# Kernel tuning notes

Hardware: AMD Instinct MI355X
Metric: run time of the kernel (lower is better)

The kernel has to match this reference:

```python
import jax, jax.numpy as jnp
import numpy as np

E, D, H, O, K = 12, 1024, 2048, 1024, 4
HH, G1, G2 = H // 2, 256, 128
B = 4096


def _ln(x, g, b):
    # torch LayerNorm over last dim, eps=1e-5
    m = x.mean(-1, keepdims=True)
    v = ((x - m) ** 2).mean(-1, keepdims=True)
    return (x - m) * jax.lax.rsqrt(v + 1e-5) * g + b


def setup_inputs() -> dict:
    key = jax.random.key(0)
    ks = jax.random.split(key, 12)
    s = 0.02
    f32 = jnp.float32
    return {
        "x": jax.random.normal(ks[0], (B, D), f32),
        # stacked expert params (E experts)
        "ew_in": jax.random.normal(ks[1], (E, D, H), f32) * s,
        "eb_in": jnp.full((E, H), 0.1, f32),
        "ln1_g": jnp.ones((E, H), f32),
        "ln1_b": jnp.zeros((E, H), f32),
        "ew_h1": jax.random.normal(ks[2], (E, H, H), f32) * s,
        "eb_h1": jnp.full((E, H), 0.1, f32),
        "ln2_g": jnp.ones((E, H), f32),
        "ln2_b": jnp.zeros((E, H), f32),
        "ew_h2": jax.random.normal(ks[3], (E, H, HH), f32) * s,
        "eb_h2": jnp.full((E, HH), 0.1, f32),
        "ew_out": jax.random.normal(ks[4], (E, HH, O), f32) * s,
        "eb_out": jnp.zeros((E, O), f32),
        # gating network params
        "gw_in": jax.random.normal(ks[5], (D, G1), f32) * s,
        "gb_in": jnp.zeros((G1,), f32),
        "gln1_g": jnp.ones((G1,), f32),
        "gln1_b": jnp.zeros((G1,), f32),
        "gw_1": jax.random.normal(ks[6], (G1, G1), f32) * s,
        "gb_1": jnp.full((G1,), 0.1, f32),
        "gln2_g": jnp.ones((G1,), f32),
        "gln2_b": jnp.zeros((G1,), f32),
        "gw_2": jax.random.normal(ks[7], (G1, G2), f32) * s,
        "gb_2": jnp.full((G2,), 0.1, f32),
        "gw_out": jax.random.normal(ks[8], (G2, E), f32) * s,
        "gb_out": jnp.zeros((E,), f32),
        "temperature": jnp.ones((1,), f32),
    }


def _moe(x, ew_in, eb_in, ln1_g, ln1_b, ew_h1, eb_h1, ln2_g, ln2_b, ew_h2,
         eb_h2, ew_out, eb_out, gw_in, gb_in, gln1_g, gln1_b, gw_1, gb_1,
         gln2_g, gln2_b, gw_2, gb_2, gw_out, gb_out, temperature):
    # ---- gating network (eval mode: no dropout / noise) ----
    g0 = jax.nn.relu(x @ gw_in + gb_in)                                # [B,256]
    g1 = jax.nn.relu(_ln(g0, gln1_g, gln1_b)) @ gw_1 + gb_1 + g0       # residual
    g2 = jax.nn.relu(_ln(g1, gln2_g, gln2_b)) @ gw_2 + gb_2            # [B,128]
    logits = (g2 @ gw_out + gb_out) / temperature                      # [B,E]
    probs = jax.nn.softmax(logits, axis=1)
    topp, topi = jax.lax.top_k(probs, K)                               # [B,K]
    topp = topp / topp.sum(axis=1, keepdims=True)
    # ---- experts: batched over E, combined with top-k one-hot weights ----
    h0 = jax.nn.relu(jnp.einsum('bd,edh->ebh', x, ew_in) + eb_in[:, None, :])
    a1 = jax.nn.relu(_ln(h0, ln1_g[:, None, :], ln1_b[:, None, :]))
    h1 = jnp.einsum('ebh,ehg->ebg', a1, ew_h1) + eb_h1[:, None, :] + h0
    a2 = jax.nn.silu(_ln(h1, ln2_g[:, None, :], ln2_b[:, None, :]))
    h2 = jnp.einsum('ebh,ehm->ebm', a2, ew_h2) + eb_h2[:, None, :]     # [E,B,H/2]
    y = jnp.einsum('ebm,emo->ebo', h2, ew_out) + eb_out[:, None, :]    # [E,B,O]
    oh = jax.nn.one_hot(topi, E, dtype=probs.dtype)                    # [B,K,E]
    w = jnp.einsum('bk,bke->be', topp, oh)                             # combine weights
    final = jnp.einsum('be,ebo->bo', w, y)                             # [B,O]
    # ---- load-balancing loss (eval-mode path) ----
    usage = probs.mean(axis=0)                                         # [E]
    ideal = 1.0 / E
    kl = jnp.sum(ideal * (jnp.log(ideal) - jnp.log(usage + 1e-8)))
    var = jnp.sum((usage - ideal) ** 2)
    ent = -jnp.sum(usage * jnp.log(usage + 1e-8))
    ent_loss = 1.0 - ent / np.log(E).astype(np.float32)
    loss = (0.5 * kl + 0.3 * var + 0.2 * ent_loss) * 0.05
    return final, loss, probs


def reference(x, ew_in, eb_in, ln1_g, ln1_b, ew_h1, eb_h1, ln2_g, ln2_b,
              ew_h2, eb_h2, ew_out, eb_out, gw_in, gb_in, gln1_g, gln1_b,
              gw_1, gb_1, gln2_g, gln2_b, gw_2, gb_2, gw_out, gb_out,
              temperature):
    return _moe(x, ew_in, eb_in, ln1_g, ln1_b, ew_h1, eb_h1, ln2_g, ln2_b,
                ew_h2, eb_h2, ew_out, eb_out, gw_in, gb_in, gln1_g, gln1_b,
                gw_1, gb_1, gln2_g, gln2_b, gw_2, gb_2, gw_out, gb_out,
                temperature)
```

## Files before the change

kernel.cpp:

```cpp
#include <hip/hip_runtime.h>
#include <cstdint>
#include <cstddef>

typedef __bf16 bf16;
typedef __bf16 bf16x4 __attribute__((ext_vector_type(4)));
typedef __bf16 bf16x8 __attribute__((ext_vector_type(8)));
typedef float  f32x4  __attribute__((ext_vector_type(4)));

#define NE   12
#define DDIM 1024
#define HDIM 2048
#define MDIM 1024
#define ODIM 1024
#define GG1  256
#define GG2  128
#define BB   4096
#define ROWS_MAX 18432

#define GPTR(p) ((const __attribute__((address_space(1))) void*)(p))
#define LPTR(p) ((__attribute__((address_space(3))) void*)(p))

__global__ void cvt_f32_bf16(const float* __restrict__ in, bf16* __restrict__ out) {
    size_t i = ((size_t)blockIdx.x * 256 + threadIdx.x) * 4;
    float4 v = *(const float4*)(in + i);
    bf16x4 o = { (bf16)v.x, (bf16)v.y, (bf16)v.z, (bf16)v.w };
    *(bf16x4*)(out + i) = o;
}

__global__ __launch_bounds__(256)
void transpose_cvt(const float* __restrict__ in, bf16* __restrict__ out,
                   int K, int N) {
    __shared__ float tile[64][65];
    const size_t eo = (size_t)blockIdx.z * K * N;
    in  += eo;
    out += eo;
    const int n0 = blockIdx.x * 64, k0 = blockIdx.y * 64;
    const int tid = threadIdx.x;

    const int rkk = tid >> 4, rnc = (tid & 15) * 4;
    #pragma unroll
    for (int p = 0; p < 4; ++p) {
        const int kk = p * 16 + rkk;
        const float4 v = *(const float4*)(in + (size_t)(k0 + kk) * N + n0 + rnc);
        tile[kk][rnc] = v.x; tile[kk][rnc + 1] = v.y;
        tile[kk][rnc + 2] = v.z; tile[kk][rnc + 3] = v.w;
    }
    __syncthreads();

    const int wnn = tid >> 3, wkc = (tid & 7) * 8;
    #pragma unroll
    for (int p = 0; p < 2; ++p) {
        const int nn = p * 32 + wnn;
        bf16x8 o;
        #pragma unroll
        for (int j = 0; j < 8; ++j) o[j] = (bf16)tile[wkc + j][nn];
        *(bf16x8*)(out + (size_t)(n0 + nn) * K + k0 + wkc) = o;
    }
}

__global__ void route_init(int* __restrict__ tok2slot, int* __restrict__ lists,
                           int* __restrict__ counts, int* __restrict__ cursors) {
    const int i = blockIdx.x * 256 + threadIdx.x;
    if (i < BB * NE)   tok2slot[i] = -1;
    if (i < ROWS_MAX)  lists[i] = 0;
    if (i < NE)        { counts[i] = 0; cursors[i] = 0; }
}

__global__ void route_count(const float* __restrict__ wcomb, int* __restrict__ counts) {
    const int t = blockIdx.x * 256 + threadIdx.x;
    const int e = blockIdx.y;
    if (wcomb[(size_t)t * NE + e] > 0.f) atomicAdd(&counts[e], 1);
}

__global__ void route_offsets(const int* __restrict__ counts, int* __restrict__ offs) {
    if (threadIdx.x == 0) {
        int o = 0;
        for (int e = 0; e < NE; ++e) { offs[e] = o; o += (counts[e] + 127) & ~127; }
        offs[NE] = o;
    }
}

__global__ void route_assign(const float* __restrict__ wcomb, const int* __restrict__ offs,
                             int* __restrict__ cursors, int* __restrict__ lists,
                             int* __restrict__ tok2slot) {
    const int t = blockIdx.x * 256 + threadIdx.x;
    const int e = blockIdx.y;
    if (wcomb[(size_t)t * NE + e] > 0.f) {
        const int pos  = atomicAdd(&cursors[e], 1);
        const int slot = offs[e] + pos;
        lists[slot] = t;
        tok2slot[(size_t)t * NE + e] = slot;
    }
}

__global__ void gather_rows(const bf16* __restrict__ xb, const int* __restrict__ lists,
                            const int* __restrict__ offs, bf16* __restrict__ xg) {
    const int e = blockIdx.y, p = blockIdx.x;
    const int off = offs[e];
    if (p >= offs[e + 1] - off) return;
    const int slot = off + p;
    const int t = lists[slot];
    const int tid = threadIdx.x;
    *(bf16x8*)&xg[(size_t)slot * DDIM + tid * 8] =
        *(const bf16x8*)&xb[(size_t)t * DDIM + tid * 8];
}

__global__ void combine_out(const int* __restrict__ tok2slot, const float* __restrict__ wcomb,
                            const float* __restrict__ yc, float* __restrict__ out) {
    const int t = blockIdx.x, tid = threadIdx.x;
    float4 acc = { 0.f, 0.f, 0.f, 0.f };
    #pragma unroll
    for (int e = 0; e < NE; ++e) {
        const int s = tok2slot[(size_t)t * NE + e];
        if (s >= 0) {
            const float w = wcomb[(size_t)t * NE + e];
            const float4 y = *(const float4*)&yc[(size_t)s * ODIM + tid * 4];
            acc.x += w * y.x; acc.y += w * y.y; acc.z += w * y.z; acc.w += w * y.w;
        }
    }
    *(float4*)&out[(size_t)t * ODIM + tid * 4] = acc;
}

template<int EPI>
__global__ __launch_bounds__(256, 2)
void egemm(const bf16* __restrict__ A, const bf16* __restrict__ Wt,
           const float* __restrict__ bias, const bf16* __restrict__ res,
           bf16* __restrict__ Cb, float* __restrict__ Cf,
           const int* __restrict__ offs, int N, int K)
{
    const int e = blockIdx.z;
    const int off  = offs[e];
    const int cntp = offs[e + 1] - off;
    const int m0 = blockIdx.y * 128;
    if (m0 >= cntp) return;
    const int n0 = blockIdx.x * 128;

    __shared__ bf16 sA[3][128 * 32];
    __shared__ bf16 sB[3][128 * 32];
    const int tid  = threadIdx.x;
    const int lane = tid & 63;
    const int wave = tid >> 6;
    const int wr = wave >> 1, wc = wave & 1;
    const int q  = lane >> 4;
    const int lr = lane & 15;

    const bf16*  Ae  = A + (size_t)off * K;
    const bf16*  Wte = Wt + (size_t)e * N * K;
    const float* be  = bias + (size_t)e * N;

    const bf16* srcA[2];
    const bf16* srcB[2];
    int dsto[2];
    #pragma unroll
    for (int i = 0; i < 2; ++i) {
        const int ch  = i * 256 + tid;
        const int row = ch >> 2, c = ch & 3;
        const int qg  = c ^ ((row >> 1) & 3);
        srcA[i] = Ae  + (size_t)(m0 + row) * K + qg * 8;
        srcB[i] = Wte + (size_t)(n0 + row) * K + qg * 8;
        dsto[i] = (i * 256 + (tid & 192)) * 8;
    }

    f32x4 acc[4][4] = {};

    auto stage = [&](int buf, int kt) {
        const int k0 = kt << 5;
        #pragma unroll
        for (int i = 0; i < 2; ++i) {
            __builtin_amdgcn_global_load_lds(GPTR(srcA[i] + k0), LPTR(&sA[buf][dsto[i]]), 16, 0, 0);
            __builtin_amdgcn_global_load_lds(GPTR(srcB[i] + k0), LPTR(&sB[buf][dsto[i]]), 16, 0, 0);
        }
    };

    const int NT = K >> 5;
    stage(0, 0);
    stage(1, 1);

    for (int kt = 0; kt < NT; ++kt) {
        const int cur = kt % 3;
        if (kt + 1 < NT) { asm volatile("s_waitcnt vmcnt(4)" ::: "memory"); }
        else             { asm volatile("s_waitcnt vmcnt(0)" ::: "memory"); }
        __builtin_amdgcn_sched_barrier(0);
        __builtin_amdgcn_s_barrier();
        __builtin_amdgcn_sched_barrier(0);

        bf16x8 fa[4], fb[4];
        #pragma unroll
        for (int mi = 0; mi < 4; ++mi) {
            const int r = wr * 64 + mi * 16 + lr;
            const int c = q ^ ((r >> 1) & 3);
            fa[mi] = *(const bf16x8*)&sA[cur][(size_t)(r * 4 + c) * 8];
        }
        #pragma unroll
        for (int ni = 0; ni < 4; ++ni) {
            const int r = wc * 64 + ni * 16 + lr;
            const int c = q ^ ((r >> 1) & 3);
            fb[ni] = *(const bf16x8*)&sB[cur][(size_t)(r * 4 + c) * 8];
        }
        #pragma unroll
        for (int mi = 0; mi < 4; ++mi)
            #pragma unroll
            for (int ni = 0; ni < 4; ++ni)
                acc[mi][ni] = __builtin_amdgcn_mfma_f32_16x16x32_bf16(fa[mi], fb[ni], acc[mi][ni], 0, 0, 0);

        if (kt + 2 < NT) stage((kt + 2) % 3, kt + 2);
    }

    #pragma unroll
    for (int ni = 0; ni < 4; ++ni) {
        const int c  = n0 + wc * 64 + ni * 16 + lr;
        const float bv = be[c];
        #pragma unroll
        for (int mi = 0; mi < 4; ++mi) {
            const int rloc = wr * 64 + mi * 16 + q * 4;
            #pragma unroll
            for (int j = 0; j < 4; ++j) {
                const size_t idx = (size_t)(off + m0 + rloc + j) * N + c;
                float v = acc[mi][ni][j] + bv;
                if constexpr (EPI == 0)      { Cb[idx] = (bf16)fmaxf(v, 0.f); }
                else if constexpr (EPI == 1) { Cb[idx] = (bf16)(v + (float)res[idx]); }
                else if constexpr (EPI == 2) { Cb[idx] = (bf16)v; }
                else                         { Cf[idx] = v; }
            }
        }
    }
}

template<int ACT>
__global__ __launch_bounds__(256)
void ln_act_bf16(const bf16* __restrict__ in, const float* __restrict__ gam,
                 const float* __restrict__ bet, bf16* __restrict__ out,
                 const int* __restrict__ offs)
{
    const int e = blockIdx.y;
    const int row = blockIdx.x;
    const int off = offs[e];
    if (row >= offs[e + 1] - off) return;
    const int tid = threadIdx.x;
    const size_t base = (size_t)(off + row) * HDIM;
    const float* g = gam + (size_t)e * HDIM;
    const float* b = bet + (size_t)e * HDIM;
    bf16x8 v = *(const bf16x8*)(in + base + tid * 8);
    float x[8], s = 0.f, ss = 0.f;
    #pragma unroll
    for (int j = 0; j < 8; ++j) { x[j] = (float)v[j]; s += x[j]; ss += x[j] * x[j]; }
    #pragma unroll
    for (int o = 1; o < 64; o <<= 1) { s += __shfl_xor(s, o); ss += __shfl_xor(ss, o); }
    __shared__ float rs[4], rss[4];
    if ((tid & 63) == 0) { rs[tid >> 6] = s; rss[tid >> 6] = ss; }
    __syncthreads();
    s  = rs[0] + rs[1] + rs[2] + rs[3];
    ss = rss[0] + rss[1] + rss[2] + rss[3];
    const float mean = s * (1.f / HDIM);
    const float var  = ss * (1.f / HDIM) - mean * mean;
    const float rstd = rsqrtf(var + 1e-5f);
    bf16x8 ov;
    #pragma unroll
    for (int j = 0; j < 8; ++j) {
        const int col = tid * 8 + j;
        float y = (x[j] - mean) * rstd * g[col] + b[col];
        if constexpr (ACT == 0) y = fmaxf(y, 0.f);
        else                    y = y / (1.f + expf(-y));
        ov[j] = (bf16)y;
    }
    *(bf16x8*)(out + base + tid * 8) = ov;
}

template<int EPI>
__global__ __launch_bounds__(256)
void gemm_f32(const float* __restrict__ A, const float* __restrict__ Bm,
              const float* __restrict__ bias, const float* __restrict__ res,
              float* __restrict__ C, int M, int N, int K)
{
    __shared__ float As[64][17];
    __shared__ float Bs[16][64];
    const int tid = threadIdx.x;
    const int tx = tid & 15, ty = tid >> 4;
    const int n0 = blockIdx.x * 64, m0 = blockIdx.y * 64;
    float acc[4][4] = {};

    for (int k0 = 0; k0 < K; k0 += 16) {
        {
            const int r = tid >> 2, c = (tid & 3) * 4;
            const float4 va = *(const float4*)(A + (size_t)(m0 + r) * K + k0 + c);
            As[r][c] = va.x; As[r][c + 1] = va.y; As[r][c + 2] = va.z; As[r][c + 3] = va.w;
            const int rb = tid >> 4, cb = (tid & 15) * 4;
            *(float4*)&Bs[rb][cb] = *(const float4*)(Bm + (size_t)(k0 + rb) * N + n0 + cb);
        }
        __syncthreads();
        #pragma unroll
        for (int k = 0; k < 16; ++k) {
            const float4 b4 = *(const float4*)&Bs[k][tx * 4];
            float av[4];
            #pragma unroll
            for (int i = 0; i < 4; ++i) av[i] = As[ty * 4 + i][k];
            #pragma unroll
            for (int i = 0; i < 4; ++i) {
                acc[i][0] += av[i] * b4.x; acc[i][1] += av[i] * b4.y;
                acc[i][2] += av[i] * b4.z; acc[i][3] += av[i] * b4.w;
            }
        }
        __syncthreads();
    }

    const float4 b4 = *(const float4*)(bias + n0 + tx * 4);
    #pragma unroll
    for (int i = 0; i < 4; ++i) {
        const int r = m0 + ty * 4 + i;
        float o[4] = { acc[i][0] + b4.x, acc[i][1] + b4.y, acc[i][2] + b4.z, acc[i][3] + b4.w };
        if constexpr (EPI == 0) {
            #pragma unroll
            for (int j = 0; j < 4; ++j) o[j] = fmaxf(o[j], 0.f);
        } else if constexpr (EPI == 1) {
            const float4 r4 = *(const float4*)(res + (size_t)r * N + n0 + tx * 4);
            o[0] += r4.x; o[1] += r4.y; o[2] += r4.z; o[3] += r4.w;
        }
        float4 o4 = { o[0], o[1], o[2], o[3] };
        *(float4*)(C + (size_t)r * N + n0 + tx * 4) = o4;
    }
}

__global__ void ln_relu_f32_256(const float* __restrict__ in, const float* __restrict__ g,
                                const float* __restrict__ b, float* __restrict__ out)
{
    const int row = blockIdx.x, lane = threadIdx.x;
    const size_t base = (size_t)row * GG1;
    const float4 v = *(const float4*)(in + base + lane * 4);
    float s  = v.x + v.y + v.z + v.w;
    float ss = v.x * v.x + v.y * v.y + v.z * v.z + v.w * v.w;
    #pragma unroll
    for (int o = 1; o < 64; o <<= 1) { s += __shfl_xor(s, o); ss += __shfl_xor(ss, o); }
    const float mean = s * (1.f / GG1);
    const float var  = ss * (1.f / GG1) - mean * mean;
    const float rstd = rsqrtf(var + 1e-5f);
    const float4 g4 = *(const float4*)(g + lane * 4);
    const float4 b4 = *(const float4*)(b + lane * 4);
    float4 o4;
    o4.x = fmaxf((v.x - mean) * rstd * g4.x + b4.x, 0.f);
    o4.y = fmaxf((v.y - mean) * rstd * g4.y + b4.y, 0.f);
    o4.z = fmaxf((v.z - mean) * rstd * g4.z + b4.z, 0.f);
    o4.w = fmaxf((v.w - mean) * rstd * g4.w + b4.w, 0.f);
    *(float4*)(out + base + lane * 4) = o4;
}

__global__ void gate_head(const float* __restrict__ g2, const float* __restrict__ gwout,
                          const float* __restrict__ gbout, const float* __restrict__ temp,
                          float* __restrict__ probs_out, float* __restrict__ wout)
{
    const int row = blockIdx.x, lane = threadIdx.x;
    __shared__ float lg[NE];
    const int e = lane >> 2, part = lane & 3;
    float acc = 0.f;
    if (e < NE) {
        const float* gr = g2 + (size_t)row * GG2;
        #pragma unroll
        for (int i = 0; i < 32; ++i) {
            const int k = part * 32 + i;
            acc += gr[k] * gwout[(size_t)k * NE + e];
        }
    }
    acc += __shfl_xor(acc, 1);
    acc += __shfl_xor(acc, 2);
    if (e < NE && part == 0) lg[e] = acc + gbout[e];
    __syncthreads();
    if (lane == 0) {
        const float t = temp[0];
        float p[NE];
        float mx = -1e30f;
        #pragma unroll
        for (int i = 0; i < NE; ++i) { p[i] = lg[i] / t; mx = fmaxf(mx, p[i]); }
        float se = 0.f;
        #pragma unroll
        for (int i = 0; i < NE; ++i) { p[i] = expf(p[i] - mx); se += p[i]; }
        const float inv = 1.f / se;
        #pragma unroll
        for (int i = 0; i < NE; ++i) { p[i] *= inv; probs_out[(size_t)row * NE + i] = p[i]; }
        float qq[NE], w[NE];
        #pragma unroll
        for (int i = 0; i < NE; ++i) { qq[i] = p[i]; w[i] = 0.f; }
        float tv[4]; int ti[4]; float tsum = 0.f;
        for (int k = 0; k < 4; ++k) {
            int best = 0; float bv = qq[0];
            for (int i = 1; i < NE; ++i) if (qq[i] > bv) { bv = qq[i]; best = i; }
            tv[k] = bv; ti[k] = best; qq[best] = -1e30f; tsum += bv;
        }
        const float it = 1.f / tsum;
        for (int k = 0; k < 4; ++k) w[ti[k]] = tv[k] * it;
        #pragma unroll
        for (int i = 0; i < NE; ++i) wout[(size_t)row * NE + i] = w[i];
    }
}

__global__ void usage_mean(const float* __restrict__ probs, float* __restrict__ usage) {
    const int e = blockIdx.x, tid = threadIdx.x;
    float s = 0.f;
    for (int r = tid; r < BB; r += 256) s += probs[(size_t)r * NE + e];
    #pragma unroll
    for (int o = 1; o < 64; o <<= 1) s += __shfl_xor(s, o);
    __shared__ float ps[4];
    if ((tid & 63) == 0) ps[tid >> 6] = s;
    __syncthreads();
    if (tid == 0) usage[e] = (ps[0] + ps[1] + ps[2] + ps[3]) / (float)BB;
}

__global__ void loss_kernel(const float* __restrict__ usage, float* __restrict__ out_loss) {
    if (threadIdx.x == 0) {
        const float ideal = 1.f / 12.f;
        float kl = 0.f, var = 0.f, ent = 0.f;
        for (int e = 0; e < NE; ++e) {
            const float u = usage[e];
            kl  += ideal * (logf(ideal) - logf(u + 1e-8f));
            var += (u - ideal) * (u - ideal);
            ent -= u * logf(u + 1e-8f);
        }
        const float entl = 1.f - ent / logf(12.f);
        out_loss[0] = (0.5f * kl + 0.3f * var + 0.2f * entl) * 0.05f;
    }
}

extern "C" void kernel_launch(void* const* d_in, const int* in_sizes, int n_in,
                              void* d_out, int out_size, void* d_ws, size_t ws_size,
                              hipStream_t stream)
{
    const float* x      = (const float*)d_in[0];
    const float* ew_in  = (const float*)d_in[1];
    const float* eb_in  = (const float*)d_in[2];
    const float* ln1_g  = (const float*)d_in[3];
    const float* ln1_b  = (const float*)d_in[4];
    const float* ew_h1  = (const float*)d_in[5];
    const float* eb_h1  = (const float*)d_in[6];
    const float* ln2_g  = (const float*)d_in[7];
    const float* ln2_b  = (const float*)d_in[8];
    const float* ew_h2  = (const float*)d_in[9];
    const float* eb_h2  = (const float*)d_in[10];
    const float* ew_out = (const float*)d_in[11];
    const float* eb_out = (const float*)d_in[12];
    const float* gw_in  = (const float*)d_in[13];
    const float* gb_in  = (const float*)d_in[14];
    const float* gln1_g = (const float*)d_in[15];
    const float* gln1_b = (const float*)d_in[16];
    const float* gw_1   = (const float*)d_in[17];
    const float* gb_1   = (const float*)d_in[18];
    const float* gln2_g = (const float*)d_in[19];
    const float* gln2_b = (const float*)d_in[20];
    const float* gw_2   = (const float*)d_in[21];
    const float* gb_2   = (const float*)d_in[22];
    const float* gw_out = (const float*)d_in[23];
    const float* gb_out = (const float*)d_in[24];
    const float* temp   = (const float*)d_in[25];

    float* out_final = (float*)d_out;
    float* out_loss  = out_final + (size_t)BB * ODIM;
    float* out_probs = out_loss + 1;

    char* ws = (char*)d_ws;
    size_t off = 0;
    auto alloc = [&](size_t bytes) -> void* {
        void* p = ws + off;
        off += (bytes + 255) & ~(size_t)255;
        return p;
    };

    bf16* xb     = (bf16*)alloc((size_t)BB * DDIM * 2);
    bf16* wt_in  = (bf16*)alloc((size_t)NE * HDIM * DDIM * 2);
    bf16* wt_h1  = (bf16*)alloc((size_t)NE * HDIM * HDIM * 2);
    bf16* wt_h2  = (bf16*)alloc((size_t)NE * MDIM * HDIM * 2);
    bf16* wt_out = (bf16*)alloc((size_t)NE * ODIM * MDIM * 2);
    bf16* xg     = (bf16*)alloc((size_t)ROWS_MAX * DDIM * 2);
    bf16* regA   = (bf16*)alloc((size_t)ROWS_MAX * HDIM * 2);
    bf16* regB   = (bf16*)alloc((size_t)ROWS_MAX * HDIM * 2);
    bf16* h1     = (bf16*)alloc((size_t)ROWS_MAX * HDIM * 2);
    float* yc    = (float*)alloc((size_t)ROWS_MAX * ODIM * 4);
    bf16* h0 = regA; bf16* a2 = regA;
    bf16* a1 = regB; bf16* h2 = regB;
    float* g0    = (float*)alloc((size_t)BB * GG1 * 4);
    float* t1    = (float*)alloc((size_t)BB * GG1 * 4);
    float* g1    = (float*)alloc((size_t)BB * GG1 * 4);
    float* t2    = (float*)alloc((size_t)BB * GG1 * 4);
    float* g2b   = (float*)alloc((size_t)BB * GG2 * 4);
    float* wcomb = (float*)alloc((size_t)BB * NE * 4);
    int*   lists = (int*)alloc((size_t)ROWS_MAX * 4);
    int*   t2s   = (int*)alloc((size_t)BB * NE * 4);
    int*   counts= (int*)alloc(256);
    int*   curs  = (int*)alloc(256);
    int*   offs  = (int*)alloc(256);
    float* usage = (float*)alloc(256);

    cvt_f32_bf16<<<dim3(BB * DDIM / 1024), dim3(256), 0, stream>>>(x, xb);
    transpose_cvt<<<dim3(HDIM / 64, DDIM / 64, NE), dim3(256), 0, stream>>>(ew_in,  wt_in,  DDIM, HDIM);
    transpose_cvt<<<dim3(HDIM / 64, HDIM / 64, NE), dim3(256), 0, stream>>>(ew_h1,  wt_h1,  HDIM, HDIM);
    transpose_cvt<<<dim3(MDIM / 64, HDIM / 64, NE), dim3(256), 0, stream>>>(ew_h2,  wt_h2,  HDIM, MDIM);
    transpose_cvt<<<dim3(ODIM / 64, MDIM / 64, NE), dim3(256), 0, stream>>>(ew_out, wt_out, MDIM, ODIM);

    gemm_f32<0><<<dim3(GG1 / 64, BB / 64), dim3(256), 0, stream>>>(x,  gw_in, gb_in, nullptr, g0,  BB, GG1, DDIM);
    ln_relu_f32_256<<<dim3(BB), dim3(64), 0, stream>>>(g0, gln1_g, gln1_b, t1);
    gemm_f32<1><<<dim3(GG1 / 64, BB / 64), dim3(256), 0, stream>>>(t1, gw_1,  gb_1,  g0,      g1,  BB, GG1, GG1);
    ln_relu_f32_256<<<dim3(BB), dim3(64), 0, stream>>>(g1, gln2_g, gln2_b, t2);
    gemm_f32<2><<<dim3(GG2 / 64, BB / 64), dim3(256), 0, stream>>>(t2, gw_2,  gb_2,  nullptr, g2b, BB, GG2, GG1);
    gate_head<<<dim3(BB), dim3(64), 0, stream>>>(g2b, gw_out, gb_out, temp, out_probs, wcomb);
    usage_mean<<<dim3(NE), dim3(256), 0, stream>>>(out_probs, usage);
    loss_kernel<<<dim3(1), dim3(64), 0, stream>>>(usage, out_loss);

    route_init<<<dim3((BB * NE + 255) / 256), dim3(256), 0, stream>>>(t2s, lists, counts, curs);
    route_count<<<dim3(BB / 256, NE), dim3(256), 0, stream>>>(wcomb, counts);
    route_offsets<<<dim3(1), dim3(64), 0, stream>>>(counts, offs);
    route_assign<<<dim3(BB / 256, NE), dim3(256), 0, stream>>>(wcomb, offs, curs, lists, t2s);
    gather_rows<<<dim3(BB, NE), dim3(128), 0, stream>>>(xb, lists, offs, xg);

    egemm<0><<<dim3(HDIM / 128, BB / 128, NE), dim3(256), 0, stream>>>(
        xg, wt_in, eb_in, nullptr, h0, nullptr, offs, HDIM, DDIM);
    ln_act_bf16<0><<<dim3(BB, NE), dim3(256), 0, stream>>>(h0, ln1_g, ln1_b, a1, offs);
    egemm<1><<<dim3(HDIM / 128, BB / 128, NE), dim3(256), 0, stream>>>(
        a1, wt_h1, eb_h1, h0, h1, nullptr, offs, HDIM, HDIM);
    ln_act_bf16<1><<<dim3(BB, NE), dim3(256), 0, stream>>>(h1, ln2_g, ln2_b, a2, offs);
    egemm<2><<<dim3(MDIM / 128, BB / 128, NE), dim3(256), 0, stream>>>(
        a2, wt_h2, eb_h2, nullptr, h2, nullptr, offs, MDIM, HDIM);
    egemm<3><<<dim3(ODIM / 128, BB / 128, NE), dim3(256), 0, stream>>>(
        h2, wt_out, eb_out, nullptr, nullptr, yc, offs, ODIM, MDIM);

    combine_out<<<dim3(BB), dim3(256), 0, stream>>>(t2s, wcomb, yc, out_final);
}
```

Baseline: 896.6 us.

## Fuse token gather into expert GEMM, deepen LDS pipeline, split-K gating GEMM

Removes the separate gather kernel by having the first expert GEMM read input rows indirectly through the routing list. Increases the GEMM software pipeline from three to four LDS stages with adjusted waitcnt thresholds. Splits the first gating GEMM over K into two partial buffers, followed by a reduction kernel that adds bias and applies ReLU. The changes trade an extra LDS footprint, which may reduce occupancy, and one extra kernel launch for fewer global memory round trips and more latency hiding.

```diff
diff --git a/kernel.cpp b/kernel.cpp
--- a/kernel.cpp
+++ b/kernel.cpp
@@ -93,18 +93,6 @@
     }
 }
 
-__global__ void gather_rows(const bf16* __restrict__ xb, const int* __restrict__ lists,
-                            const int* __restrict__ offs, bf16* __restrict__ xg) {
-    const int e = blockIdx.y, p = blockIdx.x;
-    const int off = offs[e];
-    if (p >= offs[e + 1] - off) return;
-    const int slot = off + p;
-    const int t = lists[slot];
-    const int tid = threadIdx.x;
-    *(bf16x8*)&xg[(size_t)slot * DDIM + tid * 8] =
-        *(const bf16x8*)&xb[(size_t)t * DDIM + tid * 8];
-}
-
 __global__ void combine_out(const int* __restrict__ tok2slot, const float* __restrict__ wcomb,
                             const float* __restrict__ yc, float* __restrict__ out) {
     const int t = blockIdx.x, tid = threadIdx.x;
@@ -126,7 +114,8 @@
 void egemm(const bf16* __restrict__ A, const bf16* __restrict__ Wt,
            const float* __restrict__ bias, const bf16* __restrict__ res,
            bf16* __restrict__ Cb, float* __restrict__ Cf,
-           const int* __restrict__ offs, int N, int K)
+           const int* __restrict__ offs, const int* __restrict__ lists,
+           int N, int K)
 {
     const int e = blockIdx.z;
     const int off  = offs[e];
@@ -135,8 +124,8 @@
     if (m0 >= cntp) return;
     const int n0 = blockIdx.x * 128;
 
-    __shared__ bf16 sA[3][128 * 32];
-    __shared__ bf16 sB[3][128 * 32];
+    __shared__ bf16 sA[4][128 * 32];
+    __shared__ bf16 sB[4][128 * 32];
     const int tid  = threadIdx.x;
     const int lane = tid & 63;
     const int wave = tid >> 6;
@@ -144,7 +133,6 @@
     const int q  = lane >> 4;
     const int lr = lane & 15;
 
-    const bf16*  Ae  = A + (size_t)off * K;
     const bf16*  Wte = Wt + (size_t)e * N * K;
     const float* be  = bias + (size_t)e * N;
 
@@ -156,7 +144,10 @@
         const int ch  = i * 256 + tid;
         const int row = ch >> 2, c = ch & 3;
         const int qg  = c ^ ((row >> 1) & 3);
-        srcA[i] = Ae  + (size_t)(m0 + row) * K + qg * 8;
+        size_t arow;
+        if constexpr (EPI == 0) arow = (size_t)lists[off + m0 + row];
+        else                    arow = (size_t)(off + m0 + row);
+        srcA[i] = A   + arow * K + qg * 8;
         srcB[i] = Wte + (size_t)(n0 + row) * K + qg * 8;
         dsto[i] = (i * 256 + (tid & 192)) * 8;
     }
@@ -175,11 +166,14 @@
     const int NT = K >> 5;
     stage(0, 0);
     stage(1, 1);
+    stage(2, 2);
 
     for (int kt = 0; kt < NT; ++kt) {
-        const int cur = kt % 3;
-        if (kt + 1 < NT) { asm volatile("s_waitcnt vmcnt(4)" ::: "memory"); }
-        else             { asm volatile("s_waitcnt vmcnt(0)" ::: "memory"); }
+        const int cur = kt & 3;
+        const int rem = NT - kt;
+        if (rem >= 3)      { asm volatile("s_waitcnt vmcnt(8)" ::: "memory"); }
+        else if (rem == 2) { asm volatile("s_waitcnt vmcnt(4)" ::: "memory"); }
+        else               { asm volatile("s_waitcnt vmcnt(0)" ::: "memory"); }
         __builtin_amdgcn_sched_barrier(0);
         __builtin_amdgcn_s_barrier();
         __builtin_amdgcn_sched_barrier(0);
@@ -203,7 +197,7 @@
             for (int ni = 0; ni < 4; ++ni)
                 acc[mi][ni] = __builtin_amdgcn_mfma_f32_16x16x32_bf16(fa[mi], fb[ni], acc[mi][ni], 0, 0, 0);
 
-        if (kt + 2 < NT) stage((kt + 2) % 3, kt + 2);
+        if (kt + 3 < NT) stage((kt + 3) & 3, kt + 3);
     }
 
     #pragma unroll
@@ -318,6 +312,68 @@
         float4 o4 = { o[0], o[1], o[2], o[3] };
         *(float4*)(C + (size_t)r * N + n0 + tx * 4) = o4;
     }
+}
+
+__global__ __launch_bounds__(256)
+void gemm_f32_sk(const float* __restrict__ A, const float* __restrict__ Bm,
+                 float* __restrict__ Cp, int M, int N, int K)
+{
+    __shared__ float As[64][17];
+    __shared__ float Bs[16][64];
+    const int tid = threadIdx.x;
+    const int tx = tid & 15, ty = tid >> 4;
+    const int n0 = blockIdx.x * 64, m0 = blockIdx.y * 64;
+    const int kh = K >> 1;
+    const int kb = blockIdx.z * kh, ke = kb + kh;
+    float acc[4][4] = {};
+
+    for (int k0 = kb; k0 < ke; k0 += 16) {
+        {
+            const int r = tid >> 2, c = (tid & 3) * 4;
+            const float4 va = *(const float4*)(A + (size_t)(m0 + r) * K + k0 + c);
+            As[r][c] = va.x; As[r][c + 1] = va.y; As[r][c + 2] = va.z; As[r][c + 3] = va.w;
+            const int rb = tid >> 4, cb = (tid & 15) * 4;
+            *(float4*)&Bs[rb][cb] = *(const float4*)(Bm + (size_t)(k0 + rb) * N + n0 + cb);
+        }
+        __syncthreads();
+        #pragma unroll
+        for (int k = 0; k < 16; ++k) {
+            const float4 b4 = *(const float4*)&Bs[k][tx * 4];
+            float av[4];
+            #pragma unroll
+            for (int i = 0; i < 4; ++i) av[i] = As[ty * 4 + i][k];
+            #pragma unroll
+            for (int i = 0; i < 4; ++i) {
+                acc[i][0] += av[i] * b4.x; acc[i][1] += av[i] * b4.y;
+                acc[i][2] += av[i] * b4.z; acc[i][3] += av[i] * b4.w;
+            }
+        }
+        __syncthreads();
+    }
+
+    float* Cz = Cp + (size_t)blockIdx.z * M * N;
+    #pragma unroll
+    for (int i = 0; i < 4; ++i) {
+        const int r = m0 + ty * 4 + i;
+        float4 o4 = { acc[i][0], acc[i][1], acc[i][2], acc[i][3] };
+        *(float4*)(Cz + (size_t)r * N + n0 + tx * 4) = o4;
+    }
+}
+
+__global__ void sk_reduce_relu(const float* __restrict__ Cp, const float* __restrict__ bias,
+                               float* __restrict__ C)
+{
+    const size_t i = ((size_t)blockIdx.x * 256 + threadIdx.x) * 4;
+    const int col = (int)(i % GG1);
+    const float4 a = *(const float4*)(Cp + i);
+    const float4 b = *(const float4*)(Cp + (size_t)BB * GG1 + i);
+    const float4 bi = *(const float4*)(bias + col);
+    float4 o;
+    o.x = fmaxf(a.x + b.x + bi.x, 0.f);
+    o.y = fmaxf(a.y + b.y + bi.y, 0.f);
+    o.z = fmaxf(a.z + b.z + bi.z, 0.f);
+    o.w = fmaxf(a.w + b.w + bi.w, 0.f);
+    *(float4*)(C + i) = o;
 }
 
 __global__ void ln_relu_f32_256(const float* __restrict__ in, const float* __restrict__ g,
@@ -466,13 +522,13 @@
     bf16* wt_h1  = (bf16*)alloc((size_t)NE * HDIM * HDIM * 2);
     bf16* wt_h2  = (bf16*)alloc((size_t)NE * MDIM * HDIM * 2);
     bf16* wt_out = (bf16*)alloc((size_t)NE * ODIM * MDIM * 2);
-    bf16* xg     = (bf16*)alloc((size_t)ROWS_MAX * DDIM * 2);
     bf16* regA   = (bf16*)alloc((size_t)ROWS_MAX * HDIM * 2);
     bf16* regB   = (bf16*)alloc((size_t)ROWS_MAX * HDIM * 2);
     bf16* h1     = (bf16*)alloc((size_t)ROWS_MAX * HDIM * 2);
     float* yc    = (float*)alloc((size_t)ROWS_MAX * ODIM * 4);
     bf16* h0 = regA; bf16* a2 = regA;
     bf16* a1 = regB; bf16* h2 = regB;
+    float* skbuf = (float*)alloc((size_t)2 * BB * GG1 * 4);
     float* g0    = (float*)alloc((size_t)BB * GG1 * 4);
     float* t1    = (float*)alloc((size_t)BB * GG1 * 4);
     float* g1    = (float*)alloc((size_t)BB * GG1 * 4);
@@ -492,7 +548,8 @@
     transpose_cvt<<<dim3(MDIM / 64, HDIM / 64, NE), dim3(256), 0, stream>>>(ew_h2,  wt_h2,  HDIM, MDIM);
     transpose_cvt<<<dim3(ODIM / 64, MDIM / 64, NE), dim3(256), 0, stream>>>(ew_out, wt_out, MDIM, ODIM);
 
-    gemm_f32<0><<<dim3(GG1 / 64, BB / 64), dim3(256), 0, stream>>>(x,  gw_in, gb_in, nullptr, g0,  BB, GG1, DDIM);
+    gemm_f32_sk<<<dim3(GG1 / 64, BB / 64, 2), dim3(256), 0, stream>>>(x, gw_in, skbuf, BB, GG1, DDIM);
+    sk_reduce_relu<<<dim3(BB * GG1 / 1024), dim3(256), 0, stream>>>(skbuf, gb_in, g0);
     ln_relu_f32_256<<<dim3(BB), dim3(64), 0, stream>>>(g0, gln1_g, gln1_b, t1);
     gemm_f32<1><<<dim3(GG1 / 64, BB / 64), dim3(256), 0, stream>>>(t1, gw_1,  gb_1,  g0,      g1,  BB, GG1, GG1);
     ln_relu_f32_256<<<dim3(BB), dim3(64), 0, stream>>>(g1, gln2_g, gln2_b, t2);
@@ -505,18 +562,17 @@
     route_count<<<dim3(BB / 256, NE), dim3(256), 0, stream>>>(wcomb, counts);
     route_offsets<<<dim3(1), dim3(64), 0, stream>>>(counts, offs);
     route_assign<<<dim3(BB / 256, NE), dim3(256), 0, stream>>>(wcomb, offs, curs, lists, t2s);
-    gather_rows<<<dim3(BB, NE), dim3(128), 0, stream>>>(xb, lists, offs, xg);
 
     egemm<0><<<dim3(HDIM / 128, BB / 128, NE), dim3(256), 0, stream>>>(
-        xg, wt_in, eb_in, nullptr, h0, nullptr, offs, HDIM, DDIM);
+        xb, wt_in, eb_in, nullptr, h0, nullptr, offs, lists, HDIM, DDIM);
     ln_act_bf16<0><<<dim3(BB, NE), dim3(256), 0, stream>>>(h0, ln1_g, ln1_b, a1, offs);
     egemm<1><<<dim3(HDIM / 128, BB / 128, NE), dim3(256), 0, stream>>>(
-        a1, wt_h1, eb_h1, h0, h1, nullptr, offs, HDIM, HDIM);
+        a1, wt_h1, eb_h1, h0, h1, nullptr, offs, lists, HDIM, HDIM);
     ln_act_bf16<1><<<dim3(BB, NE), dim3(256), 0, stream>>>(h1, ln2_g, ln2_b, a2, offs);
     egemm<2><<<dim3(MDIM / 128, BB / 128, NE), dim3(256), 0, stream>>>(
-        a2, wt_h2, eb_h2, nullptr, h2, nullptr, offs, MDIM, HDIM);
+        a2, wt_h2, eb_h2, nullptr, h2, nullptr, offs, lists, MDIM, HDIM);
     egemm<3><<<dim3(ODIM / 128, BB / 128, NE), dim3(256), 0, stream>>>(
-        h2, wt_out, eb_out, nullptr, nullptr, yc, offs, ODIM, MDIM);
+        h2, wt_out, eb_out, nullptr, nullptr, yc, offs, lists, ODIM, MDIM);
 
     combine_out<<<dim3(BB), dim3(256), 0, stream>>>(t2s, wcomb, yc, out_final);
 }
```

Result: slower. 928.2 us (+3.5%).
